# Kernel optimization log

Hardware: AMD Instinct MI355X
Metric: run time of the kernel (lower is better)

## Reference

```python
import jax, jax.numpy as jnp
import numpy as np

B, NPTS = 32, 2048          # batch, raw points per cloud
G, M = 128, 32              # num_group (FPS centers), group_size (KNN)
C, DEPTH, H = 384, 12, 8    # trans_dim, depth, num_heads
HD = C // H                 # head_dim = 48, divisible by 6 for 3-axis RoPE
MLP = 4 * C
CLS = 40
THETA = 100.0


def _ln(x, g, b):
    m = x.mean(-1, keepdims=True)
    v = ((x - m) ** 2).mean(-1, keepdims=True)
    return (x - m) * jax.lax.rsqrt(v + 1e-5) * g + b


def _rot_pairs(x, cos, sin):
    # rotate consecutive (even, odd) pairs of the last dim by angle arrays
    x2 = x.reshape(x.shape[:-1] + (-1, 2))
    xr, xi = x2[..., 0], x2[..., 1]
    return jnp.stack([xr * cos - xi * sin, xr * sin + xi * cos], -1).reshape(x.shape)


def _fps(pts, n):
    # farthest point sampling, first point = index 0
    Bb, N, _ = pts.shape

    def step(carry, _):
        dist, last = carry
        lp = jnp.take_along_axis(pts, last[:, None, None], axis=1)  # (B,1,3)
        dist = jnp.minimum(dist, jnp.sum((pts - lp) ** 2, -1))
        nxt = jnp.argmax(dist, -1).astype(jnp.int32)
        return (dist, nxt), last

    init = (jnp.full((Bb, N), 1e10, pts.dtype), jnp.zeros((Bb,), jnp.int32))
    _, idxs = jax.lax.scan(step, init, None, length=n)
    return idxs.T  # (B, n)


def forward(pts, enc_w1, enc_b1, enc_g1, enc_be1, enc_w2, enc_b2,
            enc_w3, enc_b3, enc_g2, enc_be2, enc_w4, enc_b4,
            cls_token, cls_pos,
            ln1_g, ln1_b, qkv_w, givens_theta, proj_w, proj_b,
            ln2_g, ln2_b, fc1_w, fc1_b, fc2_w, fc2_b,
            norm_g, norm_b,
            hw1, hb1, hg1, hbe1, hw2, hb2, hg2, hbe2, hw3, hb3):
    # ---- Group divider: FPS centers + KNN neighborhoods ----
    cidx = _fps(pts, G)
    center = jnp.take_along_axis(pts, cidx[:, :, None], axis=1)          # (B,G,3)
    d2 = jnp.sum((center[:, :, None, :] - pts[:, None, :, :]) ** 2, -1)  # (B,G,N)
    _, kidx = jax.lax.top_k(-d2, M)                                      # (B,G,M)
    neigh = jax.vmap(lambda p, i: p[i])(pts, kidx) - center[:, :, None, :]

    # ---- mini-PointNet encoder (BN in eval mode: running mean 0, var 1) ----
    x = neigh.reshape(B * G, M, 3)
    f = jax.nn.relu((x @ enc_w1.T + enc_b1) * enc_g1 + enc_be1)          # (BG,M,128)
    f = f @ enc_w2.T + enc_b2                                            # (BG,M,256)
    fg = jnp.max(f, 1, keepdims=True)
    f = jnp.concatenate([jnp.broadcast_to(fg, f.shape), f], -1)          # (BG,M,512)
    f = jax.nn.relu((f @ enc_w3.T + enc_b3) * enc_g2 + enc_be2)
    f = f @ enc_w4.T + enc_b4                                            # (BG,M,C)
    tok = jnp.max(f, 1).reshape(B, G, C)

    # ---- 3-axis axial RoPE frequencies from group centers ----
    nfr = HD // 6
    fr = 1.0 / (THETA ** (jnp.arange(nfr, dtype=pts.dtype) * 2.0 / (HD // 3)))
    ang = (center[..., None] * fr).reshape(B, G, 3 * nfr)                # (B,G,HD/2)
    pcos, psin = jnp.cos(ang)[:, None], jnp.sin(ang)[:, None]            # (B,1,G,HD/2)

    # ---- tokens: [CLS | groups] ----
    x = jnp.concatenate([jnp.broadcast_to(cls_token + cls_pos, (B, 1, C)), tok], 1)
    N = G + 1
    scale = HD ** -0.5

    for i in range(DEPTH):
        h = _ln(x, ln1_g[i], ln1_b[i])
        qkv = (h @ qkv_w[i].T).reshape(B, N, 3, H, HD).transpose(2, 0, 3, 1, 4)
        q, k, v = qkv[0], qkv[1], qkv[2]                                 # (B,H,N,HD)
        # learnable Givens rotation (per-head block-diagonal pair rotations)
        gcos = jnp.cos(givens_theta[i])[None, :, None]                   # (1,H,1,HD/2)
        gsin = jnp.sin(givens_theta[i])[None, :, None]
        q = _rot_pairs(q, gcos, gsin)
        k = _rot_pairs(k, gcos, gsin)
        # positional RoPE on non-CLS tokens only
        q = jnp.concatenate([q[:, :, :1], _rot_pairs(q[:, :, 1:], pcos, psin)], 2)
        k = jnp.concatenate([k[:, :, :1], _rot_pairs(k[:, :, 1:], pcos, psin)], 2)
        attn = jax.nn.softmax(jnp.einsum('bhqd,bhkd->bhqk', q, k) * scale, -1)
        o = jnp.einsum('bhqk,bhkd->bhqd', attn, v).transpose(0, 2, 1, 3).reshape(B, N, C)
        x = x + o @ proj_w[i].T + proj_b[i]
        h = _ln(x, ln2_g[i], ln2_b[i])
        x = x + jax.nn.gelu(h @ fc1_w[i].T + fc1_b[i], approximate=False) @ fc2_w[i].T + fc2_b[i]

    x = _ln(x, norm_g, norm_b)
    feat = jnp.concatenate([x[:, 0], jnp.max(x[:, 1:], 1)], -1)          # (B,2C)
    hfe = jax.nn.relu((feat @ hw1.T + hb1) * hg1 + hbe1)
    hfe = jax.nn.relu((hfe @ hw2.T + hb2) * hg2 + hbe2)
    return hfe @ hw3.T + hb3                                             # (B,CLS)


def setup_inputs() -> dict:
    key = jax.random.key(0)
    ks = iter(jax.random.split(key, 64))
    nrm = lambda *s: jax.random.normal(next(ks), s, jnp.float32) * 0.02
    d = dict(
        pts=jax.random.normal(next(ks), (B, NPTS, 3), jnp.float32),
        enc_w1=nrm(128, 3), enc_b1=jnp.zeros(128), enc_g1=jnp.ones(128), enc_be1=jnp.zeros(128),
        enc_w2=nrm(256, 128), enc_b2=jnp.zeros(256),
        enc_w3=nrm(512, 512), enc_b3=jnp.zeros(512), enc_g2=jnp.ones(512), enc_be2=jnp.zeros(512),
        enc_w4=nrm(C, 512), enc_b4=jnp.zeros(C),
        cls_token=nrm(1, 1, C), cls_pos=nrm(1, 1, C),
        ln1_g=jnp.ones((DEPTH, C)), ln1_b=jnp.zeros((DEPTH, C)),
        qkv_w=nrm(DEPTH, 3 * C, C), givens_theta=nrm(DEPTH, H, HD // 2),
        proj_w=nrm(DEPTH, C, C), proj_b=jnp.zeros((DEPTH, C)),
        ln2_g=jnp.ones((DEPTH, C)), ln2_b=jnp.zeros((DEPTH, C)),
        fc1_w=nrm(DEPTH, MLP, C), fc1_b=jnp.zeros((DEPTH, MLP)),
        fc2_w=nrm(DEPTH, C, MLP), fc2_b=jnp.zeros((DEPTH, C)),
        norm_g=jnp.ones(C), norm_b=jnp.zeros(C),
        hw1=nrm(256, 2 * C), hb1=jnp.zeros(256), hg1=jnp.ones(256), hbe1=jnp.zeros(256),
        hw2=nrm(256, 256), hb2=jnp.zeros(256), hg2=jnp.ones(256), hbe2=jnp.zeros(256),
        hw3=nrm(CLS, 256), hb3=jnp.zeros(CLS),
    )
    return d


def reference(pts, enc_w1, enc_b1, enc_g1, enc_be1, enc_w2, enc_b2,
              enc_w3, enc_b3, enc_g2, enc_be2, enc_w4, enc_b4,
              cls_token, cls_pos,
              ln1_g, ln1_b, qkv_w, givens_theta, proj_w, proj_b,
              ln2_g, ln2_b, fc1_w, fc1_b, fc2_w, fc2_b,
              norm_g, norm_b,
              hw1, hb1, hg1, hbe1, hw2, hb2, hg2, hbe2, hw3, hb3):
    return forward(pts, enc_w1, enc_b1, enc_g1, enc_be1, enc_w2, enc_b2,
                   enc_w3, enc_b3, enc_g2, enc_be2, enc_w4, enc_b4,
                   cls_token, cls_pos,
                   ln1_g, ln1_b, qkv_w, givens_theta, proj_w, proj_b,
                   ln2_g, ln2_b, fc1_w, fc1_b, fc2_w, fc2_b,
                   norm_g, norm_b,
                   hw1, hb1, hg1, hbe1, hw2, hb2, hg2, hbe2, hw3, hb3)
```

## Files before the change

kernel.cpp:

```cpp
#include <hip/hip_runtime.h>
#include <math.h>

constexpr int kB   = 32;
constexpr int kN   = 2048;
constexpr int kG   = 128;
constexpr int kM   = 32;
constexpr int kC   = 384;
constexpr int kH   = 8;
constexpr int kHD  = 48;
constexpr int kNT  = 129;
constexpr int kMLP = 1536;
constexpr int kRows = kB * kNT;
constexpr int kGC  = 512;
constexpr int kRC  = kGC * kM;

typedef __attribute__((ext_vector_type(8))) short bf16x8;
typedef __attribute__((ext_vector_type(4))) float f32x4;

__device__ __forceinline__ unsigned short f2bf(float x) {
  unsigned u = __float_as_uint(x);
  unsigned r = (u + 0x7fffu + ((u >> 16) & 1u)) >> 16;
  return (unsigned short)r;
}
__device__ __forceinline__ float bf2f(unsigned short u) {
  return __uint_as_float(((unsigned)u) << 16);
}

__global__ __launch_bounds__(64, 1) void fps_kernel(
    const float* __restrict__ pts, float* __restrict__ center)
{
  #pragma clang fp contract(off)
  __shared__ float sx[kN + 64], sy[kN + 64], sz[kN + 64];
  const int b = blockIdx.x, lane = threadIdx.x;
  const float* P = pts + (size_t)b * kN * 3;
  float rx[32], ry[32], rz[32], rd[32];
  const int base = lane * 32;
  #pragma unroll
  for (int j = 0; j < 32; ++j) {
    int i = base + j;
    float x = P[3*i], y = P[3*i+1], z = P[3*i+2];
    rx[j] = x; ry[j] = y; rz[j] = z; rd[j] = 1e10f;
    int ii = lane*33 + j;
    sx[ii] = x; sy[ii] = y; sz[ii] = z;
  }
  __syncthreads();
  int last = 0;
  float* cb = center + (size_t)b * kG * 3;
  for (int it = 0; it < kG; ++it) {
    int ls = last + (last >> 5);
    float lx = sx[ls], ly = sy[ls], lz = sz[ls];
    if (lane == 0) { cb[3*it] = lx; cb[3*it+1] = ly; cb[3*it+2] = lz; }
    float bestv = -1.0f; int besti = kN;
    #pragma unroll
    for (int j = 0; j < 32; ++j) {
      float dx = rx[j]-lx, dy = ry[j]-ly, dz = rz[j]-lz;
      float d = (dx*dx + dy*dy) + dz*dz;
      float nd = fminf(rd[j], d);
      rd[j] = nd;
      if (nd > bestv) { bestv = nd; besti = base + j; }
    }
    #pragma unroll
    for (int off = 1; off < 64; off <<= 1) {
      float vv = __shfl_xor(bestv, off);
      int   ii = __shfl_xor(besti, off);
      if (vv > bestv || (vv == bestv && ii < besti)) { bestv = vv; besti = ii; }
    }
    last = besti;
  }
}

__global__ void rope_kernel(const float* __restrict__ center,
                            float* __restrict__ pcs, float* __restrict__ psn)
{
  int idx = blockIdx.x*256 + threadIdx.x;
  if (idx >= kB*kG*24) return;
  int p  = idx % 24;
  int bg = idx / 24;
  int axis = p >> 3, j = p & 7;
  float e  = (float)(2*j) / 16.0f;
  float fr = 1.0f / powf(100.0f, e);
  float ang = center[(size_t)bg*3 + axis] * fr;
  pcs[idx] = cosf(ang);
  psn[idx] = sinf(ang);
}

__global__ __launch_bounds__(256) void knn_kernel(
    const float* __restrict__ pts, const float* __restrict__ center,
    float* __restrict__ neigh)
{
  #pragma clang fp contract(off)
  __shared__ float sx[kN + kN/32], sy[kN + kN/32], sz[kN + kN/32];
  const int t = threadIdx.x;
  const int lane = t & 63, w = t >> 6;
  const int blk = blockIdx.x;
  const int b = blk >> 5;
  const float* P = pts + (size_t)b * kN * 3;
  for (int i = t; i < kN; i += 256) {
    int ii = i + (i >> 5);
    sx[ii] = P[3*i]; sy[ii] = P[3*i+1]; sz[ii] = P[3*i+2];
  }
  __syncthreads();
  const int bg = b*kG + (blk & 31)*4 + w;
  const float cx = center[(size_t)bg*3+0];
  const float cy = center[(size_t)bg*3+1];
  const float cz = center[(size_t)bg*3+2];
  float rd[32];
  const int base = lane * 32;
  #pragma unroll
  for (int j = 0; j < 32; ++j) {
    int is = lane*33 + j;
    float dx = cx - sx[is], dy = cy - sy[is], dz = cz - sz[is];
    rd[j] = (dx*dx + dy*dy) + dz*dz;
  }
  float* ob = neigh + (size_t)bg * kM * 3;
  int lastWin = -1;
  for (int m = 0; m < kM; ++m) {
    float bestv = 3.0e38f; int besti = kN;
    #pragma unroll
    for (int j = 0; j < 32; ++j) {
      float v = rd[j];
      if (base + j == lastWin) v = 3.0e38f;
      rd[j] = v;
      if (v < bestv) { bestv = v; besti = base + j; }
    }
    #pragma unroll
    for (int off = 1; off < 64; off <<= 1) {
      float vv = __shfl_xor(bestv, off);
      int   i2 = __shfl_xor(besti, off);
      if (vv < bestv || (vv == bestv && i2 < besti)) { bestv = vv; besti = i2; }
    }
    lastWin = besti;
    if (lane == 0) {
      int is = besti + (besti >> 5);
      ob[3*m+0] = sx[is] - cx; ob[3*m+1] = sy[is] - cy; ob[3*m+2] = sz[is] - cz;
    }
  }
}

__global__ void wcvt_kernel(const float* __restrict__ s,
                            unsigned short* __restrict__ d, int n)
{
  int i = (blockIdx.x*256 + threadIdx.x)*8;
  if (i >= n) return;
  float4 a = *(const float4*)(s + i), b = *(const float4*)(s + i + 4);
  bf16x8 v;
  v[0]=(short)f2bf(a.x); v[1]=(short)f2bf(a.y); v[2]=(short)f2bf(a.z); v[3]=(short)f2bf(a.w);
  v[4]=(short)f2bf(b.x); v[5]=(short)f2bf(b.y); v[6]=(short)f2bf(b.z); v[7]=(short)f2bf(b.w);
  *(bf16x8*)(d + i) = v;
}

__global__ void wcvt4_kernel(const float* __restrict__ q, const float* __restrict__ p,
                             const float* __restrict__ f1, const float* __restrict__ f2,
                             unsigned short* __restrict__ d)
{
  int i = (blockIdx.x*256 + threadIdx.x)*8;
  const float* s; int lo;
  if (i < 442368)       { s = q;  lo = i; }
  else if (i < 589824)  { s = p;  lo = i - 442368; }
  else if (i < 1179648) { s = f1; lo = i - 589824; }
  else                  { s = f2; lo = i - 1179648; }
  float4 a = *(const float4*)(s + lo), b = *(const float4*)(s + lo + 4);
  bf16x8 v;
  v[0]=(short)f2bf(a.x); v[1]=(short)f2bf(a.y); v[2]=(short)f2bf(a.z); v[3]=(short)f2bf(a.w);
  v[4]=(short)f2bf(b.x); v[5]=(short)f2bf(b.y); v[6]=(short)f2bf(b.z); v[7]=(short)f2bf(b.w);
  *(bf16x8*)(d + i) = v;
}

__global__ __launch_bounds__(256) void enc1_kernel(
    const float* __restrict__ neighC,
    const float* __restrict__ w1, const float* __restrict__ b1,
    const float* __restrict__ g1, const float* __restrict__ be1,
    unsigned short* __restrict__ f1c)
{
  const int t = threadIdx.x;
  const int r = blockIdx.x*2 + (t >> 7);
  const int c = t & 127;
  const float* nr = neighC + (size_t)r*3;
  float x0 = nr[0], x1 = nr[1], x2 = nr[2];
  float s = x0*w1[3*c] + x1*w1[3*c+1] + x2*w1[3*c+2] + b1[c];
  float v = fmaxf(s*g1[c] + be1[c], 0.0f);
  f1c[(size_t)r*128 + c] = f2bf(v);
}

__global__ __launch_bounds__(256) void pool2_kernel(
    const unsigned short* __restrict__ f2c, unsigned short* __restrict__ fgc)
{
  const int g = blockIdx.x, c = threadIdx.x;
  float mx = -3.0e38f;
  #pragma unroll 8
  for (int m = 0; m < kM; ++m)
    mx = fmaxf(mx, bf2f(f2c[((size_t)g*kM + m)*256 + c]));
  fgc[(size_t)g*256 + c] = f2bf(mx);
}

template <int EPI, int FM, int FN>
__global__ __launch_bounds__(256) void mgemm_kernel(
    const unsigned short* __restrict__ A, int lda,
    const unsigned short* __restrict__ Bb, int ldb,
    void* __restrict__ Cv,
    const float* __restrict__ bias,
    const float* __restrict__ aux,
    const float* __restrict__ gsc, const float* __restrict__ bsc,
    int Mm, int Nn, int Kk,
    float* __restrict__ poolOut, int poolG0)
{
  constexpr int BM = FM*32, BN = FN*32;
  __shared__ unsigned short As[BM][72];
  __shared__ unsigned short Bs[BN][72];
  const int t = threadIdx.x;
  const int m0 = blockIdx.x * BM;
  const int n0 = blockIdx.y * BN;
  const int w = t >> 6, lane = t & 63;
  const int wm = w >> 1, wn = w & 1;
  const int lr = lane & 15;
  const int lk = (lane >> 4) * 8;
  const int srow = t >> 3;
  const int skseg = (t & 7) * 8;
  f32x4 acc[FM][FN] = {};
  for (int k0 = 0; k0 < Kk; k0 += 64) {
    #pragma unroll
    for (int p = 0; p < BM/32; ++p) {
      int r = p*32 + srow;
      int gr = m0 + r;
      bf16x8 av = {};
      if (gr < Mm) av = *(const bf16x8*)(A + (size_t)gr*lda + k0 + skseg);
      *(bf16x8*)(&As[r][skseg]) = av;
    }
    #pragma unroll
    for (int p = 0; p < BN/32; ++p) {
      int r = p*32 + srow;
      bf16x8 bv = *(const bf16x8*)(Bb + (size_t)(n0 + r)*ldb + k0 + skseg);
      *(bf16x8*)(&Bs[r][skseg]) = bv;
    }
    __syncthreads();
    #pragma unroll
    for (int kk = 0; kk < 64; kk += 32) {
      bf16x8 af[FM], bf[FN];
      #pragma unroll
      for (int i = 0; i < FM; ++i)
        af[i] = *(const bf16x8*)(&As[wm*(FM*16) + i*16 + lr][kk + lk]);
      #pragma unroll
      for (int i = 0; i < FN; ++i)
        bf[i] = *(const bf16x8*)(&Bs[wn*(FN*16) + i*16 + lr][kk + lk]);
      #pragma unroll
      for (int i = 0; i < FM; ++i)
        #pragma unroll
        for (int j = 0; j < FN; ++j)
          acc[i][j] = __builtin_amdgcn_mfma_f32_16x16x32_bf16(af[i], bf[j], acc[i][j], 0, 0, 0);
    }
    __syncthreads();
  }

  if constexpr (EPI == 4) {
    #pragma unroll
    for (int ni = 0; ni < FN; ++ni) {
      int cc = n0 + wn*(FN*16) + ni*16 + lr;
      float mx = -3.0e38f;
      #pragma unroll
      for (int mi = 0; mi < FM; ++mi)
        #pragma unroll
        for (int j = 0; j < 4; ++j)
          mx = fmaxf(mx, acc[mi][ni][j]);
      mx = fmaxf(mx, __shfl_xor(mx, 16));
      mx = fmaxf(mx, __shfl_xor(mx, 32));
      if ((lane >> 4) == 0) {
        int ggl = poolG0 + (m0 >> 5) + wm;
        int b = ggl >> 7, g = ggl & 127;
        poolOut[((size_t)b*kNT + 1 + g)*kC + cc] = mx + bias[cc];
      }
    }
    return;
  }

  #pragma unroll
  for (int mi = 0; mi < FM; ++mi) {
    #pragma unroll
    for (int j = 0; j < 4; ++j) {
      int r = m0 + wm*(FM*16) + mi*16 + (lane >> 4)*4 + j;
      if (r < Mm) {
        #pragma unroll
        for (int ni = 0; ni < FN; ++ni) {
          int cc = n0 + wn*(FN*16) + ni*16 + lr;
          float v = acc[mi][ni][j];
          size_t o = (size_t)r*Nn + cc;
          if constexpr (EPI == 0) {
            ((unsigned short*)Cv)[o] = f2bf(v);
          } else if constexpr (EPI == 1) {
            ((unsigned short*)Cv)[o] = f2bf(v + bias[cc]);
          } else if constexpr (EPI == 2) {
            ((float*)Cv)[o] = v + bias[cc];
          } else if constexpr (EPI == 3) {
            float u = (v + aux[(size_t)(r >> 5)*Nn + cc])*gsc[cc] + bsc[cc];
            ((unsigned short*)Cv)[o] = f2bf(fmaxf(u, 0.0f));
          } else if constexpr (EPI == 5) {
            ((float*)Cv)[o] = aux[o] + v + bias[cc];
          } else {
            float u = v + bias[cc];
            ((unsigned short*)Cv)[o] = f2bf(0.5f*u*(1.0f + erff(u*0.70710678118654752440f)));
          }
        }
      }
    }
  }
}

__global__ void cls_kernel(const float* __restrict__ ct, const float* __restrict__ cp,
                           float* __restrict__ x)
{
  int idx = blockIdx.x*256 + threadIdx.x;
  if (idx >= kB*kC) return;
  int b = idx / kC, c = idx % kC;
  x[(size_t)b*kNT*kC + c] = ct[c] + cp[c];
}

template <int OUTBF>
__global__ __launch_bounds__(256) void ln_kernel(
    const float* __restrict__ in, void* __restrict__ outv,
    const float* __restrict__ g, const float* __restrict__ bb)
{
  const int t = threadIdx.x;
  const int lane = t & 63;
  const int row = blockIdx.x*4 + (t >> 6);
  const float* p = in + (size_t)row*kC;
  float v[6];
  #pragma unroll
  for (int k = 0; k < 6; ++k) v[k] = p[k*64 + lane];
  float s = 0.f;
  #pragma unroll
  for (int k = 0; k < 6; ++k) s += v[k];
  #pragma unroll
  for (int off = 1; off < 64; off <<= 1) s += __shfl_xor(s, off);
  float mean = s / 384.0f;
  float vs = 0.f;
  #pragma unroll
  for (int k = 0; k < 6; ++k) { float d = v[k]-mean; vs += d*d; }
  #pragma unroll
  for (int off = 1; off < 64; off <<= 1) vs += __shfl_xor(vs, off);
  float r = rsqrtf(vs / 384.0f + 1e-5f);
  #pragma unroll
  for (int k = 0; k < 6; ++k) {
    int c = k*64 + lane;
    float o = (v[k]-mean)*r*g[c] + bb[c];
    if constexpr (OUTBF) ((unsigned short*)outv)[(size_t)row*kC + c] = f2bf(o);
    else                 ((float*)outv)[(size_t)row*kC + c] = o;
  }
}

__global__ __launch_bounds__(512) void attn_kernel(
    const unsigned short* __restrict__ qkv, const float* __restrict__ pcs,
    const float* __restrict__ psn, const float* __restrict__ gth,
    unsigned short* __restrict__ o)
{
  __shared__ float qs[kNT][kHD];
  __shared__ float ks[kNT][kHD];
  __shared__ float vls[kNT][kHD];
  __shared__ float gcs[24], gss[24];
  __shared__ float ps[8][132];
  const int t = threadIdx.x;
  const int bh = blockIdx.x;
  const int b = bh >> 3, hh = bh & 7;
  if (t < 24) { float th = gth[hh*24 + t]; gcs[t] = cosf(th); gss[t] = sinf(th); }
  __syncthreads();
  for (int idx = t; idx < kNT*24; idx += 512) {
    int n = idx / 24, p = idx % 24;
    const unsigned short* base = qkv + ((size_t)(b*kNT + n))*1152 + hh*kHD + 2*p;
    float q0 = bf2f(base[0]),   q1 = bf2f(base[1]);
    float k0 = bf2f(base[384]), k1 = bf2f(base[385]);
    float v0 = bf2f(base[768]), v1 = bf2f(base[769]);
    float cg = gcs[p], sg = gss[p];
    float qr = q0*cg - q1*sg, qi = q0*sg + q1*cg;
    float kr = k0*cg - k1*sg, ki = k0*sg + k1*cg;
    if (n > 0) {
      size_t pi = ((size_t)b*kG + (n-1))*24 + p;
      float pc = pcs[pi], pv = psn[pi];
      float tq = qr*pc - qi*pv; qi = qr*pv + qi*pc; qr = tq;
      float tk = kr*pc - ki*pv; ki = kr*pv + ki*pc; kr = tk;
    }
    qs[n][2*p] = qr; qs[n][2*p+1] = qi;
    ks[n][2*p] = kr; ks[n][2*p+1] = ki;
    vls[n][2*p] = v0; vls[n][2*p+1] = v1;
  }
  __syncthreads();
  const int lane = t & 63, w = t >> 6;
  for (int r = w; r < kNT; r += 8) {
    float4 q[12];
    #pragma unroll
    for (int d = 0; d < 12; ++d) q[d] = *(const float4*)(&qs[r][d*4]);
    float sv[3];
    float mx = -3.0e38f;
    #pragma unroll
    for (int ji = 0; ji < 3; ++ji) {
      int j = ji*64 + lane;
      float s = -3.0e38f;
      if (j < kNT) {
        float a0 = 0.f, a1 = 0.f;
        #pragma unroll
        for (int d = 0; d < 12; d += 2) {
          float4 k0v = *(const float4*)(&ks[j][d*4]);
          float4 k1v = *(const float4*)(&ks[j][d*4+4]);
          a0 += q[d].x*k0v.x + q[d].y*k0v.y + q[d].z*k0v.z + q[d].w*k0v.w;
          a1 += q[d+1].x*k1v.x + q[d+1].y*k1v.y + q[d+1].z*k1v.z + q[d+1].w*k1v.w;
        }
        s = (a0 + a1) * 0.14433756729740643f;
      }
      sv[ji] = s;
      mx = fmaxf(mx, s);
    }
    #pragma unroll
    for (int off = 1; off < 64; off <<= 1) mx = fmaxf(mx, __shfl_xor(mx, off));
    float sum = 0.f;
    #pragma unroll
    for (int ji = 0; ji < 3; ++ji) {
      int j = ji*64 + lane;
      if (j < kNT) { float e = expf(sv[ji] - mx); ps[w][j] = e; sum += e; }
    }
    #pragma unroll
    for (int off = 1; off < 64; off <<= 1) sum += __shfl_xor(sum, off);
    if (lane < kHD) {
      float ac0 = 0.f, ac1 = 0.f, ac2 = 0.f, ac3 = 0.f;
      for (int j4 = 0; j4 < 128; j4 += 16) {
        float4 p0 = *(const float4*)(&ps[w][j4]);
        float4 p1 = *(const float4*)(&ps[w][j4+4]);
        float4 p2 = *(const float4*)(&ps[w][j4+8]);
        float4 p3 = *(const float4*)(&ps[w][j4+12]);
        ac0 += p0.x*vls[j4+0][lane] + p0.y*vls[j4+1][lane]
             + p0.z*vls[j4+2][lane] + p0.w*vls[j4+3][lane];
        ac1 += p1.x*vls[j4+4][lane] + p1.y*vls[j4+5][lane]
             + p1.z*vls[j4+6][lane] + p1.w*vls[j4+7][lane];
        ac2 += p2.x*vls[j4+8][lane] + p2.y*vls[j4+9][lane]
             + p2.z*vls[j4+10][lane] + p2.w*vls[j4+11][lane];
        ac3 += p3.x*vls[j4+12][lane] + p3.y*vls[j4+13][lane]
             + p3.z*vls[j4+14][lane] + p3.w*vls[j4+15][lane];
      }
      float accv = ((ac0 + ac1) + (ac2 + ac3)) + ps[w][128]*vls[128][lane];
      o[((size_t)(b*kNT + r))*kC + hh*kHD + lane] = f2bf(accv / sum);
    }
  }
}

__global__ __launch_bounds__(256) void head_kernel(
    const float* __restrict__ xf,
    const float* __restrict__ hw1, const float* __restrict__ hb1,
    const float* __restrict__ hg1, const float* __restrict__ hbe1,
    const float* __restrict__ hw2, const float* __restrict__ hb2,
    const float* __restrict__ hg2, const float* __restrict__ hbe2,
    const float* __restrict__ hw3, const float* __restrict__ hb3,
    float* __restrict__ out)
{
  __shared__ float f[768];
  __shared__ float h1[256], h2[256];
  const int t = threadIdx.x;
  const int b = blockIdx.x;
  const float* xb = xf + (size_t)b*kNT*kC;
  for (int c = t; c < kC; c += 256) {
    f[c] = xb[c];
    float mx = -3.0e38f;
    for (int n = 1; n < kNT; ++n) mx = fmaxf(mx, xb[(size_t)n*kC + c]);
    f[kC + c] = mx;
  }
  __syncthreads();
  {
    float acc = hb1[t];
    for (int k = 0; k < 768; k += 4) {
      float4 wv = *(const float4*)(hw1 + (size_t)t*768 + k);
      float4 fv = *(const float4*)(&f[k]);
      acc += fv.x*wv.x + fv.y*wv.y + fv.z*wv.z + fv.w*wv.w;
    }
    h1[t] = fmaxf(acc*hg1[t] + hbe1[t], 0.0f);
  }
  __syncthreads();
  {
    float acc = hb2[t];
    for (int k = 0; k < 256; k += 4) {
      float4 wv = *(const float4*)(hw2 + (size_t)t*256 + k);
      float4 fv = *(const float4*)(&h1[k]);
      acc += fv.x*wv.x + fv.y*wv.y + fv.z*wv.z + fv.w*wv.w;
    }
    h2[t] = fmaxf(acc*hg2[t] + hbe2[t], 0.0f);
  }
  __syncthreads();
  if (t < 40) {
    float acc = hb3[t];
    for (int k = 0; k < 256; k += 4) {
      float4 wv = *(const float4*)(hw3 + (size_t)t*256 + k);
      float4 fv = *(const float4*)(&h2[k]);
      acc += fv.x*wv.x + fv.y*wv.y + fv.z*wv.z + fv.w*wv.w;
    }
    out[(size_t)b*40 + t] = acc;
  }
}

extern "C" void kernel_launch(void* const* d_in, const int* in_sizes, int n_in,
                              void* d_out, int out_size, void* d_ws, size_t ws_size,
                              hipStream_t stream) {
  const float* pts     = (const float*)d_in[0];
  const float* enc_w1  = (const float*)d_in[1];
  const float* enc_b1  = (const float*)d_in[2];
  const float* enc_g1  = (const float*)d_in[3];
  const float* enc_be1 = (const float*)d_in[4];
  const float* enc_w2  = (const float*)d_in[5];
  const float* enc_b2  = (const float*)d_in[6];
  const float* enc_w3  = (const float*)d_in[7];
  const float* enc_b3  = (const float*)d_in[8];
  const float* enc_g2  = (const float*)d_in[9];
  const float* enc_be2 = (const float*)d_in[10];
  const float* enc_w4  = (const float*)d_in[11];
  const float* enc_b4  = (const float*)d_in[12];
  const float* cls_tok = (const float*)d_in[13];
  const float* cls_pos = (const float*)d_in[14];
  const float* ln1_g   = (const float*)d_in[15];
  const float* ln1_b   = (const float*)d_in[16];
  const float* qkv_w   = (const float*)d_in[17];
  const float* givens  = (const float*)d_in[18];
  const float* proj_w  = (const float*)d_in[19];
  const float* proj_b  = (const float*)d_in[20];
  const float* ln2_g   = (const float*)d_in[21];
  const float* ln2_b   = (const float*)d_in[22];
  const float* fc1_w   = (const float*)d_in[23];
  const float* fc1_b   = (const float*)d_in[24];
  const float* fc2_w   = (const float*)d_in[25];
  const float* fc2_b   = (const float*)d_in[26];
  const float* norm_g  = (const float*)d_in[27];
  const float* norm_b  = (const float*)d_in[28];
  const float* hw1     = (const float*)d_in[29];
  const float* hb1     = (const float*)d_in[30];
  const float* hg1     = (const float*)d_in[31];
  const float* hbe1    = (const float*)d_in[32];
  const float* hw2     = (const float*)d_in[33];
  const float* hb2     = (const float*)d_in[34];
  const float* hg2     = (const float*)d_in[35];
  const float* hbe2    = (const float*)d_in[36];
  const float* hw3     = (const float*)d_in[37];
  const float* hb3     = (const float*)d_in[38];

  constexpr size_t kWL = 1769472ull;
  char* wsb = (char*)d_ws;
  size_t off = 0;
  float* center = (float*)(wsb + off); off += (size_t)kB*kG*3*4;
  float* pcs    = (float*)(wsb + off); off += (size_t)kB*kG*24*4;
  float* psn    = (float*)(wsb + off); off += (size_t)kB*kG*24*4;
  float* neigh  = (float*)(wsb + off); off += (size_t)kB*kG*kM*3*4;
  float* xbuf   = (float*)(wsb + off); off += (size_t)kRows*kC*4;
  unsigned short* encwb = (unsigned short*)(wsb + off); off += 491520ull*2;
  unsigned short* wlbf  = (unsigned short*)(wsb + off);
  const size_t scratchNeed = 16777216ull + 8388608ull + 262144ull + 1048576ull;
  const bool bigws = ws_size >= off + 12*kWL*2 + scratchNeed;
  off += (bigws ? 12*kWL*2 : kWL*2);
  char* scratch = wsb + off;
  unsigned short* f3c   = (unsigned short*)(scratch);
  unsigned short* f1c   = (unsigned short*)(scratch);
  unsigned short* f2c   = (unsigned short*)(scratch + 16777216);
  unsigned short* fgc   = (unsigned short*)(scratch + 16777216 + 8388608);
  float*          basec = (float*)(scratch + 16777216 + 8388608 + 262144);
  unsigned short* hbuf   = (unsigned short*)(scratch);
  unsigned short* qkvb   = (unsigned short*)(scratch + 3170304);
  unsigned short* attnob = (unsigned short*)(scratch + 3170304 + 9510912);
  unsigned short* mlpb   = (unsigned short*)(scratch + 3170304);
  float*          flnb   = (float*)(scratch + 3170304);

  const unsigned short* encw2 = encwb;
  const unsigned short* encw3 = encwb + 32768;
  const unsigned short* encw4 = encwb + 32768 + 262144;

  fps_kernel<<<kB, 64, 0, stream>>>(pts, center);
  rope_kernel<<<(kB*kG*24 + 255)/256, 256, 0, stream>>>(center, pcs, psn);
  knn_kernel<<<kB*kG/4, 256, 0, stream>>>(pts, center, neigh);

  wcvt_kernel<<<32768/8/256, 256, 0, stream>>>(enc_w2, (unsigned short*)encw2, 32768);
  wcvt_kernel<<<262144/8/256, 256, 0, stream>>>(enc_w3, (unsigned short*)encw3, 262144);
  wcvt_kernel<<<196608/8/256, 256, 0, stream>>>(enc_w4, (unsigned short*)encw4, 196608);
  if (bigws) {
    for (int l = 0; l < 12; ++l)
      wcvt4_kernel<<<864, 256, 0, stream>>>(
          qkv_w + (size_t)l*442368, proj_w + (size_t)l*147456,
          fc1_w + (size_t)l*589824, fc2_w + (size_t)l*589824, wlbf + (size_t)l*kWL);
  }

  for (int c = 0; c < 8; ++c) {
    const float* nc = neigh + (size_t)c*kRC*3;
    enc1_kernel<<<kRC/2, 256, 0, stream>>>(nc, enc_w1, enc_b1, enc_g1, enc_be1, f1c);
    mgemm_kernel<1,2,2><<<dim3(kRC/64, 4), 256, 0, stream>>>(
        f1c, 128, encw2, 128, f2c, enc_b2, nullptr, nullptr, nullptr,
        kRC, 256, 128, nullptr, 0);
    pool2_kernel<<<kGC, 256, 0, stream>>>(f2c, fgc);
    mgemm_kernel<2,2,2><<<dim3(kGC/64, 8), 256, 0, stream>>>(
        fgc, 256, encw3, 512, basec, enc_b3, nullptr, nullptr, nullptr,
        kGC, 512, 256, nullptr, 0);
    mgemm_kernel<3,2,2><<<dim3(kRC/64, 8), 256, 0, stream>>>(
        f2c, 256, encw3 + 256, 512, f3c, nullptr, basec, enc_g2, enc_be2,
        kRC, 512, 256, nullptr, 0);
    mgemm_kernel<4,2,2><<<dim3(kRC/64, 6), 256, 0, stream>>>(
        f3c, 512, encw4, 512, nullptr, enc_b4, nullptr, nullptr, nullptr,
        kRC, 384, 512, xbuf, c*kGC);
  }
  cls_kernel<<<(kB*kC + 255)/256, 256, 0, stream>>>(cls_tok, cls_pos, xbuf);

  const int lnGrid = kRows/4;
  for (int l = 0; l < 12; ++l) {
    unsigned short* wl = wlbf + (bigws ? (size_t)l*kWL : 0);
    if (!bigws)
      wcvt4_kernel<<<864, 256, 0, stream>>>(
          qkv_w + (size_t)l*442368, proj_w + (size_t)l*147456,
          fc1_w + (size_t)l*589824, fc2_w + (size_t)l*589824, wl);
    const unsigned short* wq  = wl;
    const unsigned short* wp  = wl + 442368;
    const unsigned short* w1f = wl + 589824;
    const unsigned short* w2f = wl + 1179648;
    ln_kernel<1><<<lnGrid, 256, 0, stream>>>(xbuf, hbuf, ln1_g + l*kC, ln1_b + l*kC);
    mgemm_kernel<0,2,2><<<dim3(65, 18), 256, 0, stream>>>(
        hbuf, kC, wq, kC, qkvb, nullptr, nullptr, nullptr, nullptr,
        kRows, 1152, kC, nullptr, 0);
    attn_kernel<<<kB*kH, 512, 0, stream>>>(qkvb, pcs, psn, givens + (size_t)l*kH*24, attnob);
    mgemm_kernel<5,2,2><<<dim3(65, 6), 256, 0, stream>>>(
        attnob, kC, wp, kC, xbuf, proj_b + l*kC, xbuf, nullptr, nullptr,
        kRows, kC, kC, nullptr, 0);
    ln_kernel<1><<<lnGrid, 256, 0, stream>>>(xbuf, hbuf, ln2_g + l*kC, ln2_b + l*kC);
    mgemm_kernel<6,2,2><<<dim3(65, 24), 256, 0, stream>>>(
        hbuf, kC, w1f, kC, mlpb, fc1_b + l*kMLP, nullptr, nullptr, nullptr,
        kRows, kMLP, kC, nullptr, 0);
    mgemm_kernel<5,2,2><<<dim3(65, 6), 256, 0, stream>>>(
        mlpb, kMLP, w2f, kMLP, xbuf, fc2_b + l*kC, xbuf, nullptr, nullptr,
        kRows, kC, kMLP, nullptr, 0);
  }
  ln_kernel<0><<<lnGrid, 256, 0, stream>>>(xbuf, flnb, norm_g, norm_b);
  head_kernel<<<kB, 256, 0, stream>>>(flnb,
      hw1, hb1, hg1, hbe1, hw2, hb2, hg2, hbe2, hw3, hb3, (float*)d_out);
}
```

Measured before the change: 2.411 ms.

## Parallelize FPS over 256 threads, widen GEMM N tiles, pad attention K smem

FPS now runs with 256 threads, 8 points each, instead of one wavefront holding 32 points per lane. The argmax winner's coordinates travel through the shuffle reduction and a cross-wave shared-memory step, which removes the shared-memory point lookup. Several GEMM launches switch to a wider N tile (template 2,4, half the grid in y) to get more reuse per block, and the attention K tile is padded to 52 floats to avoid LDS bank conflicts. The risks are two block barriers per FPS iteration and more register pressure and fewer blocks for the GEMMs.

Measured after the change: 2.627 ms. +9.0%, slower.

```diff
diff --git a/kernel.cpp b/kernel.cpp
--- a/kernel.cpp
+++ b/kernel.cpp
@@ -26,46 +26,61 @@
   return __uint_as_float(((unsigned)u) << 16);
 }
 
-__global__ __launch_bounds__(64, 1) void fps_kernel(
+__global__ __launch_bounds__(256) void fps_kernel(
     const float* __restrict__ pts, float* __restrict__ center)
 {
   #pragma clang fp contract(off)
-  __shared__ float sx[kN + 64], sy[kN + 64], sz[kN + 64];
-  const int b = blockIdx.x, lane = threadIdx.x;
+  __shared__ float rvv[4], rxx[4], ryy[4], rzz[4];
+  __shared__ int   rii[4];
+  const int b = blockIdx.x, t = threadIdx.x;
+  const int lane = t & 63, w = t >> 6;
   const float* P = pts + (size_t)b * kN * 3;
-  float rx[32], ry[32], rz[32], rd[32];
-  const int base = lane * 32;
-  #pragma unroll
-  for (int j = 0; j < 32; ++j) {
+  float rx[8], ry[8], rz[8], rd[8];
+  const int base = t * 8;
+  #pragma unroll
+  for (int j = 0; j < 8; ++j) {
     int i = base + j;
-    float x = P[3*i], y = P[3*i+1], z = P[3*i+2];
-    rx[j] = x; ry[j] = y; rz[j] = z; rd[j] = 1e10f;
-    int ii = lane*33 + j;
-    sx[ii] = x; sy[ii] = y; sz[ii] = z;
-  }
-  __syncthreads();
-  int last = 0;
+    rx[j] = P[3*i]; ry[j] = P[3*i+1]; rz[j] = P[3*i+2];
+    rd[j] = 1e10f;
+  }
+  float lx = P[0], ly = P[1], lz = P[2];
   float* cb = center + (size_t)b * kG * 3;
   for (int it = 0; it < kG; ++it) {
-    int ls = last + (last >> 5);
-    float lx = sx[ls], ly = sy[ls], lz = sz[ls];
-    if (lane == 0) { cb[3*it] = lx; cb[3*it+1] = ly; cb[3*it+2] = lz; }
+    if (t == 0) { cb[3*it] = lx; cb[3*it+1] = ly; cb[3*it+2] = lz; }
     float bestv = -1.0f; int besti = kN;
-    #pragma unroll
-    for (int j = 0; j < 32; ++j) {
+    float bx = 0.f, by = 0.f, bz = 0.f;
+    #pragma unroll
+    for (int j = 0; j < 8; ++j) {
       float dx = rx[j]-lx, dy = ry[j]-ly, dz = rz[j]-lz;
       float d = (dx*dx + dy*dy) + dz*dz;
       float nd = fminf(rd[j], d);
       rd[j] = nd;
-      if (nd > bestv) { bestv = nd; besti = base + j; }
+      if (nd > bestv) { bestv = nd; besti = base + j; bx = rx[j]; by = ry[j]; bz = rz[j]; }
     }
     #pragma unroll
     for (int off = 1; off < 64; off <<= 1) {
       float vv = __shfl_xor(bestv, off);
       int   ii = __shfl_xor(besti, off);
-      if (vv > bestv || (vv == bestv && ii < besti)) { bestv = vv; besti = ii; }
-    }
-    last = besti;
+      float xx = __shfl_xor(bx, off);
+      float yy = __shfl_xor(by, off);
+      float zz = __shfl_xor(bz, off);
+      if (vv > bestv || (vv == bestv && ii < besti)) {
+        bestv = vv; besti = ii; bx = xx; by = yy; bz = zz;
+      }
+    }
+    if (lane == 0) { rvv[w] = bestv; rii[w] = besti; rxx[w] = bx; ryy[w] = by; rzz[w] = bz; }
+    __syncthreads();
+    float v = rvv[0]; int bi = rii[0];
+    float nx = rxx[0], ny = ryy[0], nz = rzz[0];
+    #pragma unroll
+    for (int k = 1; k < 4; ++k) {
+      float vk = rvv[k]; int ik = rii[k];
+      if (vk > v || (vk == v && ik < bi)) {
+        v = vk; bi = ik; nx = rxx[k]; ny = ryy[k]; nz = rzz[k];
+      }
+    }
+    lx = nx; ly = ny; lz = nz;
+    __syncthreads();
   }
 }
 
@@ -352,7 +367,7 @@
     unsigned short* __restrict__ o)
 {
   __shared__ float qs[kNT][kHD];
-  __shared__ float ks[kNT][kHD];
+  __shared__ float ks[kNT][52];
   __shared__ float vls[kNT][kHD];
   __shared__ float gcs[24], gss[24];
   __shared__ float ps[8][132];
@@ -562,7 +577,7 @@
   const unsigned short* encw3 = encwb + 32768;
   const unsigned short* encw4 = encwb + 32768 + 262144;
 
-  fps_kernel<<<kB, 64, 0, stream>>>(pts, center);
+  fps_kernel<<<kB, 256, 0, stream>>>(pts, center);
   rope_kernel<<<(kB*kG*24 + 255)/256, 256, 0, stream>>>(center, pcs, psn);
   knn_kernel<<<kB*kG/4, 256, 0, stream>>>(pts, center, neigh);
 
@@ -579,17 +594,17 @@
   for (int c = 0; c < 8; ++c) {
     const float* nc = neigh + (size_t)c*kRC*3;
     enc1_kernel<<<kRC/2, 256, 0, stream>>>(nc, enc_w1, enc_b1, enc_g1, enc_be1, f1c);
-    mgemm_kernel<1,2,2><<<dim3(kRC/64, 4), 256, 0, stream>>>(
+    mgemm_kernel<1,2,4><<<dim3(kRC/64, 2), 256, 0, stream>>>(
         f1c, 128, encw2, 128, f2c, enc_b2, nullptr, nullptr, nullptr,
         kRC, 256, 128, nullptr, 0);
     pool2_kernel<<<kGC, 256, 0, stream>>>(f2c, fgc);
     mgemm_kernel<2,2,2><<<dim3(kGC/64, 8), 256, 0, stream>>>(
         fgc, 256, encw3, 512, basec, enc_b3, nullptr, nullptr, nullptr,
         kGC, 512, 256, nullptr, 0);
-    mgemm_kernel<3,2,2><<<dim3(kRC/64, 8), 256, 0, stream>>>(
+    mgemm_kernel<3,2,4><<<dim3(kRC/64, 4), 256, 0, stream>>>(
         f2c, 256, encw3 + 256, 512, f3c, nullptr, basec, enc_g2, enc_be2,
         kRC, 512, 256, nullptr, 0);
-    mgemm_kernel<4,2,2><<<dim3(kRC/64, 6), 256, 0, stream>>>(
+    mgemm_kernel<4,2,4><<<dim3(kRC/64, 3), 256, 0, stream>>>(
         f3c, 512, encw4, 512, nullptr, enc_b4, nullptr, nullptr, nullptr,
         kRC, 384, 512, xbuf, c*kGC);
   }
@@ -607,7 +622,7 @@
     const unsigned short* w1f = wl + 589824;
     const unsigned short* w2f = wl + 1179648;
     ln_kernel<1><<<lnGrid, 256, 0, stream>>>(xbuf, hbuf, ln1_g + l*kC, ln1_b + l*kC);
-    mgemm_kernel<0,2,2><<<dim3(65, 18), 256, 0, stream>>>(
+    mgemm_kernel<0,2,4><<<dim3(65, 9), 256, 0, stream>>>(
         hbuf, kC, wq, kC, qkvb, nullptr, nullptr, nullptr, nullptr,
         kRows, 1152, kC, nullptr, 0);
     attn_kernel<<<kB*kH, 512, 0, stream>>>(qkvb, pcs, psn, givens + (size_t)l*kH*24, attnob);
@@ -615,7 +630,7 @@
         attnob, kC, wp, kC, xbuf, proj_b + l*kC, xbuf, nullptr, nullptr,
         kRows, kC, kC, nullptr, 0);
     ln_kernel<1><<<lnGrid, 256, 0, stream>>>(xbuf, hbuf, ln2_g + l*kC, ln2_b + l*kC);
-    mgemm_kernel<6,2,2><<<dim3(65, 24), 256, 0, stream>>>(
+    mgemm_kernel<6,2,4><<<dim3(65, 12), 256, 0, stream>>>(
         hbuf, kC, w1f, kC, mlpb, fc1_b + l*kMLP, nullptr, nullptr, nullptr,
         kRows, kMLP, kC, nullptr, 0);
     mgemm_kernel<5,2,2><<<dim3(65, 6), 256, 0, stream>>>(
```
